# Kernel tuning notes

Measured on AMD Instinct MI355X. Metric: run time of the kernel, lower is better.

The kernel has to match this reference:

```python
import jax, jax.numpy as jnp
import numpy as np
from jax import lax

DIM = 64
K = 3
GROUPS = 1
NUM_KERNELS = 4
B, H, W = 32, 128, 128


def setup_inputs() -> dict:
    key = jax.random.key(0)
    k1, k2, k3, k4 = jax.random.split(key, 4)
    x = jax.random.normal(k1, (B, DIM, H, W), dtype=jnp.float32)
    attention = jax.random.uniform(k2, (B, NUM_KERNELS), dtype=jnp.float32)
    # kaiming-uniform-like init per kernel: bound = sqrt(6 / fan_in)
    fan_in = (DIM // GROUPS) * K * K
    bound = float(np.sqrt(6.0 / fan_in))
    weight = jax.random.uniform(k3, (NUM_KERNELS, DIM, DIM // GROUPS, K, K),
                                dtype=jnp.float32, minval=-bound, maxval=bound)
    bias_p = jax.random.normal(k4, (NUM_KERNELS, DIM), dtype=jnp.float32) * 0.1
    return {"x": x, "attention": attention, "weight": weight, "bias_p": bias_p}


def reference(x, attention, weight, bias_p):
    # Mix kernel bank per sample: [B, nk] @ [nk, dim*dim//g*k*k]
    w_flat = weight.reshape(NUM_KERNELS, -1)
    w_mix = (attention @ w_flat).reshape(B, DIM, DIM // GROUPS, K, K)
    b_mix = attention @ bias_p  # [B, dim]

    def conv_one(xb, wb, bb):
        # xb: [C,H,W], wb: [C_out, C_in//g, k, k]
        out = lax.conv_general_dilated(
            xb[None], wb, window_strides=(1, 1), padding="SAME",
            dimension_numbers=("NCHW", "OIHW", "NCHW"),
            feature_group_count=GROUPS)
        return out[0] + bb[:, None, None]

    return jax.vmap(conv_one)(x, w_mix, b_mix)  # [B, dim, H, W]
```

## Files before the change

### kernel.cpp

```cpp
#include <hip/hip_runtime.h>


#define DIM 64
#define BATCH 32
#define HH 128
#define WW 128
#define NK 4

typedef __attribute__((ext_vector_type(4))) float f32x4;
typedef __attribute__((ext_vector_type(8))) short bf16x8;
typedef __attribute__((ext_vector_type(8))) unsigned short ushort8;

static __device__ __forceinline__ unsigned short f2bf(float f) {
    union { float f; unsigned u; } v; v.f = f;
    unsigned r = v.u + 0x7fffu + ((v.u >> 16) & 1u);
    return (unsigned short)(r >> 16);
}
static __device__ __forceinline__ unsigned pack2(float a, float b) {
    return (unsigned)f2bf(a) | ((unsigned)f2bf(b) << 16);
}

__global__ __launch_bounds__(256) void mix_weights(
    const float* __restrict__ w, const float* __restrict__ att,
    unsigned short* __restrict__ wmix) {
    __shared__ float tr[4][576];
    int wave = threadIdx.x >> 6, lane = threadIdx.x & 63;
    int idx = blockIdx.x * 4 + wave;
    int b = idx >> 6, co = idx & 63;
    float a[NK];
    #pragma unroll
    for (int k = 0; k < NK; ++k) a[k] = att[b * NK + k];
    float s[9];
    #pragma unroll
    for (int t = 0; t < 9; ++t) s[t] = 0.f;
    #pragma unroll
    for (int k = 0; k < NK; ++k) {
        const float* wp = w + (size_t)(k * DIM + co) * 576;
        #pragma unroll
        for (int t = 0; t < 9; ++t)
            s[t] += a[k] * wp[t * 64 + lane];
    }
    #pragma unroll
    for (int t = 0; t < 9; ++t) tr[wave][t * 64 + lane] = s[t];
    __syncthreads();
    int mt = co >> 4;
    int lo = ((lane >> 3) & 3) * 16 + (co & 15);
    int ss = lane >> 5;
    int jj = lane & 7;
    #pragma unroll
    for (int t = 0; t < 9; ++t) {
        float v = tr[wave][lane * 9 + t];
        wmix[(size_t)((((b * 9 + t) * 2 + ss) * 4 + mt) * 64 + lo) * 8 + jj] = f2bf(v);
    }
}

__global__ __launch_bounds__(256) void mix_bias(
    const float* __restrict__ bias, const float* __restrict__ att,
    float* __restrict__ bmix) {
    int idx = blockIdx.x * 256 + threadIdx.x;
    if (idx >= BATCH * DIM) return;
    int b = idx >> 6, co = idx & 63;
    float s = 0.f;
    for (int k = 0; k < NK; ++k) s += att[b * NK + k] * bias[k * DIM + co];
    bmix[idx] = s;
}

__global__ __launch_bounds__(256, 3) void conv_mfma(
    const float* __restrict__ x, const unsigned short* __restrict__ wmix,
    const float* __restrict__ bmix, float* __restrict__ out) {

    __shared__ unsigned short Xs[6 * 66 * 64];

    int bid = blockIdx.x;
    bid = (bid & 7) * 256 + (bid >> 3);
    int b   = bid >> 6;
    int r6  = bid & 63;
    int h0  = (r6 >> 1) * 4;
    int w0  = (r6 & 1) * 64;

    int tid  = threadIdx.x;
    int wave = tid >> 6, lane = tid & 63;
    int l15  = lane & 15, q = lane >> 4;

    #pragma unroll
    for (int half = 0; half < 2; ++half) {
        f32x4 xv[3][2][2];
        #pragma unroll
        for (int rr = 0; rr < 3; ++rr) {
            int r = half * 3 + rr;
            int hin = h0 - 1 + r;
            bool ok = (hin >= 0) && (hin < HH);
            #pragma unroll
            for (int it = 0; it < 2; ++it) {
                int slot = it * 256 + tid;
                int p = slot >> 4, c4 = slot & 15;
                f32x4 z = {0.f, 0.f, 0.f, 0.f};
                xv[rr][it][0] = ok ? *(const f32x4*)&x[(((size_t)b * DIM + 2 * p    ) * HH + hin) * WW + w0 + c4 * 4] : z;
                xv[rr][it][1] = ok ? *(const f32x4*)&x[(((size_t)b * DIM + 2 * p + 1) * HH + hin) * WW + w0 + c4 * 4] : z;
            }
        }
        #pragma unroll
        for (int rr = 0; rr < 3; ++rr) {
            int r = half * 3 + rr;
            #pragma unroll
            for (int it = 0; it < 2; ++it) {
                int slot = it * 256 + tid;
                int p = slot >> 4, c4 = slot & 15;
                #pragma unroll
                for (int j = 0; j < 4; ++j) {
                    int c = c4 * 4 + 1 + j;
                    int xi = (r * 66 + c) * 64 + (((p >> 2) ^ ((c >> 1) & 7)) << 3) + 2 * (p & 3);
                    *(unsigned*)&Xs[xi] = pack2(xv[rr][it][0][j], xv[rr][it][1][j]);
                }
            }
        }
    }
    #pragma unroll
    for (int e = 0; e < 3; ++e) {
        int item = e * 256 + tid;
        int edge = item >= 384;
        int jj = item - edge * 384;
        int ci = jj & 63, r = jj >> 6;
        int hin = h0 - 1 + r;
        int win = edge ? (w0 + 64) : (w0 - 1);
        float v = 0.f;
        if (hin >= 0 && hin < HH && win >= 0 && win < WW)
            v = x[(((size_t)b * DIM + ci) * HH + hin) * WW + win];
        int c = edge ? 65 : 0;
        Xs[(r * 66 + c) * 64 + (((ci >> 3) ^ ((c >> 1) & 7)) << 3) + (ci & 7)] = f2bf(v);
    }

    const unsigned short* wa = wmix + (size_t)b * 9 * 4096;
    bf16x8 afp[4];
    #pragma unroll
    for (int mt = 0; mt < 4; ++mt)
        afp[mt] = *(const bf16x8*)&wa[(size_t)(mt * 64 + lane) * 8];

    f32x4 acc[4][4];
    f32x4 zero = {0.f, 0.f, 0.f, 0.f};
    #pragma unroll
    for (int mt = 0; mt < 4; ++mt)
        #pragma unroll
        for (int nt = 0; nt < 4; ++nt) acc[mt][nt] = zero;

    __syncthreads();

    #pragma unroll
    for (int tap = 0; tap < 9; ++tap) {
        int kh = tap / 3, kw = tap - kh * 3;
        int r = wave + kh;
        #pragma unroll
        for (int s = 0; s < 2; ++s) {
            int u = tap * 2 + s;
            bf16x8 afc[4];
            #pragma unroll
            for (int mt = 0; mt < 4; ++mt) afc[mt] = afp[mt];
            if (u < 17) {
                #pragma unroll
                for (int mt = 0; mt < 4; ++mt)
                    afp[mt] = *(const bf16x8*)&wa[(size_t)(((u + 1) * 4 + mt) * 64 + lane) * 8];
            }
            int g = s * 4 + q;
            bf16x8 bfr[4];
            #pragma unroll
            for (int nt = 0; nt < 4; ++nt) {
                int c = nt * 16 + l15 + kw;
                bfr[nt] = *(const bf16x8*)&Xs[(r * 66 + c) * 64 + ((g ^ ((c >> 1) & 7)) << 3)];
            }
            #pragma unroll
            for (int mt = 0; mt < 4; ++mt)
                #pragma unroll
                for (int nt = 0; nt < 4; ++nt)
                    acc[mt][nt] = __builtin_amdgcn_mfma_f32_16x16x32_bf16(
                        afc[mt], bfr[nt], acc[mt][nt], 0, 0, 0);
        }
    }

    float biasr[4][4];
    #pragma unroll
    for (int mt = 0; mt < 4; ++mt)
        #pragma unroll
        for (int rg = 0; rg < 4; ++rg)
            biasr[mt][rg] = bmix[b * DIM + mt * 16 + q * 4 + rg];
    int h = h0 + wave;
    #pragma unroll
    for (int mt = 0; mt < 4; ++mt) {
        #pragma unroll
        for (int nt = 0; nt < 4; ++nt) {
            int wcol = w0 + nt * 16 + l15;
            #pragma unroll
            for (int rg = 0; rg < 4; ++rg) {
                int co = mt * 16 + q * 4 + rg;
                out[(((size_t)b * DIM + co) * HH + h) * WW + wcol] = acc[mt][nt][rg] + biasr[mt][rg];
            }
        }
    }
}

extern "C" void kernel_launch(void* const* d_in, const int* in_sizes, int n_in,
                              void* d_out, int out_size, void* d_ws, size_t ws_size,
                              hipStream_t stream) {
    const float* x   = (const float*)d_in[0];
    const float* att = (const float*)d_in[1];
    const float* wgt = (const float*)d_in[2];
    const float* bia = (const float*)d_in[3];
    float* out = (float*)d_out;

    unsigned short* wmix = (unsigned short*)d_ws;
    float* bmix = (float*)((char*)d_ws + 2359296);

    mix_weights<<<512, 256, 0, stream>>>(wgt, att, wmix);
    mix_bias<<<8, 256, 0, stream>>>(bia, att, bmix);
    conv_mfma<<<2048, 256, 0, stream>>>(x, wmix, bmix, out);
}
```

Measured before the change: 268.8 us.

## Deepen weight prefetch to three stages and widen LDS staging stores

Weight fragments are now prefetched three steps ahead in a rotating triple buffer, and the first three are issued before the input staging loads so their latency overlaps the tile fill. Input staging is reorganized so each thread loads four consecutive channels and writes 8-byte packed stores to LDS instead of 4-byte ones, halving the LDS store count. This costs more VGPRs for the extra weight buffers, which could pressure the occupancy target of three blocks per SIMD.

```diff
diff --git a/kernel.cpp b/kernel.cpp
--- a/kernel.cpp
+++ b/kernel.cpp
@@ -10,6 +10,7 @@
 typedef __attribute__((ext_vector_type(4))) float f32x4;
 typedef __attribute__((ext_vector_type(8))) short bf16x8;
 typedef __attribute__((ext_vector_type(8))) unsigned short ushort8;
+typedef __attribute__((ext_vector_type(2))) unsigned int u32x2;
 
 static __device__ __forceinline__ unsigned short f2bf(float f) {
     union { float f; unsigned u; } v; v.f = f;
@@ -82,36 +83,40 @@
     int wave = tid >> 6, lane = tid & 63;
     int l15  = lane & 15, q = lane >> 4;
 
+    const unsigned short* wa = wmix + (size_t)b * 9 * 4096;
+    bf16x8 afp[3][4];
+    #pragma unroll
+    for (int u0 = 0; u0 < 3; ++u0)
+        #pragma unroll
+        for (int mt = 0; mt < 4; ++mt)
+            afp[u0][mt] = *(const bf16x8*)&wa[(size_t)((u0 * 4 + mt) * 64 + lane) * 8];
+
+    int cq = tid >> 4, c4 = tid & 15;
     #pragma unroll
     for (int half = 0; half < 2; ++half) {
-        f32x4 xv[3][2][2];
+        f32x4 xv[3][4];
         #pragma unroll
         for (int rr = 0; rr < 3; ++rr) {
             int r = half * 3 + rr;
             int hin = h0 - 1 + r;
             bool ok = (hin >= 0) && (hin < HH);
             #pragma unroll
-            for (int it = 0; it < 2; ++it) {
-                int slot = it * 256 + tid;
-                int p = slot >> 4, c4 = slot & 15;
+            for (int i = 0; i < 4; ++i) {
                 f32x4 z = {0.f, 0.f, 0.f, 0.f};
-                xv[rr][it][0] = ok ? *(const f32x4*)&x[(((size_t)b * DIM + 2 * p    ) * HH + hin) * WW + w0 + c4 * 4] : z;
-                xv[rr][it][1] = ok ? *(const f32x4*)&x[(((size_t)b * DIM + 2 * p + 1) * HH + hin) * WW + w0 + c4 * 4] : z;
+                xv[rr][i] = ok ? *(const f32x4*)&x[(((size_t)b * DIM + 4 * cq + i) * HH + hin) * WW + w0 + 4 * c4] : z;
             }
         }
         #pragma unroll
         for (int rr = 0; rr < 3; ++rr) {
             int r = half * 3 + rr;
             #pragma unroll
-            for (int it = 0; it < 2; ++it) {
-                int slot = it * 256 + tid;
-                int p = slot >> 4, c4 = slot & 15;
-                #pragma unroll
-                for (int j = 0; j < 4; ++j) {
-                    int c = c4 * 4 + 1 + j;
-                    int xi = (r * 66 + c) * 64 + (((p >> 2) ^ ((c >> 1) & 7)) << 3) + 2 * (p & 3);
-                    *(unsigned*)&Xs[xi] = pack2(xv[rr][it][0][j], xv[rr][it][1][j]);
-                }
+            for (int j = 0; j < 4; ++j) {
+                int c = 4 * c4 + 1 + j;
+                u32x2 pk;
+                pk.x = pack2(xv[rr][0][j], xv[rr][1][j]);
+                pk.y = pack2(xv[rr][2][j], xv[rr][3][j]);
+                int xi = (r * 66 + c) * 64 + (((cq >> 1) ^ ((c >> 1) & 7)) << 3) + 4 * (cq & 1);
+                *(u32x2*)&Xs[xi] = pk;
             }
         }
     }
@@ -130,12 +135,6 @@
         Xs[(r * 66 + c) * 64 + (((ci >> 3) ^ ((c >> 1) & 7)) << 3) + (ci & 7)] = f2bf(v);
     }
 
-    const unsigned short* wa = wmix + (size_t)b * 9 * 4096;
-    bf16x8 afp[4];
-    #pragma unroll
-    for (int mt = 0; mt < 4; ++mt)
-        afp[mt] = *(const bf16x8*)&wa[(size_t)(mt * 64 + lane) * 8];
-
     f32x4 acc[4][4];
     f32x4 zero = {0.f, 0.f, 0.f, 0.f};
     #pragma unroll
@@ -146,33 +145,27 @@
     __syncthreads();
 
     #pragma unroll
-    for (int tap = 0; tap < 9; ++tap) {
+    for (int u = 0; u < 18; ++u) {
+        int tap = u >> 1, s = u & 1;
         int kh = tap / 3, kw = tap - kh * 3;
         int r = wave + kh;
-        #pragma unroll
-        for (int s = 0; s < 2; ++s) {
-            int u = tap * 2 + s;
-            bf16x8 afc[4];
-            #pragma unroll
-            for (int mt = 0; mt < 4; ++mt) afc[mt] = afp[mt];
-            if (u < 17) {
-                #pragma unroll
-                for (int mt = 0; mt < 4; ++mt)
-                    afp[mt] = *(const bf16x8*)&wa[(size_t)(((u + 1) * 4 + mt) * 64 + lane) * 8];
-            }
-            int g = s * 4 + q;
-            bf16x8 bfr[4];
-            #pragma unroll
-            for (int nt = 0; nt < 4; ++nt) {
-                int c = nt * 16 + l15 + kw;
-                bfr[nt] = *(const bf16x8*)&Xs[(r * 66 + c) * 64 + ((g ^ ((c >> 1) & 7)) << 3)];
-            }
+        int g = s * 4 + q;
+        bf16x8 bfr[4];
+        #pragma unroll
+        for (int nt = 0; nt < 4; ++nt) {
+            int c = nt * 16 + l15 + kw;
+            bfr[nt] = *(const bf16x8*)&Xs[(r * 66 + c) * 64 + ((g ^ ((c >> 1) & 7)) << 3)];
+        }
+        #pragma unroll
+        for (int mt = 0; mt < 4; ++mt)
+            #pragma unroll
+            for (int nt = 0; nt < 4; ++nt)
+                acc[mt][nt] = __builtin_amdgcn_mfma_f32_16x16x32_bf16(
+                    afp[u % 3][mt], bfr[nt], acc[mt][nt], 0, 0, 0);
+        if (u + 3 < 18) {
             #pragma unroll
             for (int mt = 0; mt < 4; ++mt)
-                #pragma unroll
-                for (int nt = 0; nt < 4; ++nt)
-                    acc[mt][nt] = __builtin_amdgcn_mfma_f32_16x16x32_bf16(
-                        afc[mt], bfr[nt], acc[mt][nt], 0, 0, 0);
+                afp[u % 3][mt] = *(const bf16x8*)&wa[(size_t)(((u + 3) * 4 + mt) * 64 + lane) * 8];
         }
     }
 
```

New measurement: 271.8 us. About the same (+1.1%).
